# Optimization experiments

Measured on AMD Instinct MI355X. Metric: run time of the kernel, lower is better.

The kernel has to match this reference:

```python
import math
import jax, jax.numpy as jnp
import numpy as np

NUM_HEADS = 16
HEAD_DIM = 128  # hidden_size 2048 / 16 heads


def setup_inputs() -> dict:
    key = jax.random.key(0)
    kq, kk, kv = jax.random.split(key, 3)
    B, S, D = 2, 2048, 2048
    return {
        "query": jax.random.normal(kq, (B, S, D), dtype=jnp.float32),
        "key": jax.random.normal(kk, (B, S, D), dtype=jnp.float32),
        "value": jax.random.normal(kv, (B, S, D), dtype=jnp.float32),
        "attention_mask": jnp.zeros((B, 1, 1, S), dtype=jnp.float32),
    }


def reference(query, key, value, attention_mask):
    B, S, D = query.shape
    H, hd = NUM_HEADS, HEAD_DIM
    # [B, S, D] -> [B, H, S, hd]
    q = query.reshape(B, S, H, hd).transpose(0, 2, 1, 3)
    k = key.reshape(B, S, H, hd).transpose(0, 2, 1, 3)
    v = value.reshape(B, S, H, hd).transpose(0, 2, 1, 3)
    scale = 1.0 / math.sqrt(hd)
    # scores: [B, H, S, S]
    scores = jnp.einsum("bhqd,bhkd->bhqk", q, k) * scale
    scores = scores + attention_mask  # additive broadcastable mask
    attn_weights = jax.nn.softmax(scores, axis=-1)
    # dropout p=0.0 / eval mode -> no-op
    attn_output = jnp.einsum("bhqk,bhkd->bhqd", attn_weights, v)
    attn_output = attn_output.transpose(0, 2, 1, 3).reshape(B, S, D)
    return (attn_output, attn_weights)
```

## Files before the change

kernel.cpp:

```cpp
#include <hip/hip_runtime.h>

#define SQ 2048
#define DM 2048
#define NH 16
#define HD 128
#define NB 2
#define NBH 32

typedef __attribute__((ext_vector_type(8))) short bf16x8;
typedef __attribute__((ext_vector_type(4))) float f32x4;

__device__ __forceinline__ unsigned short f2bf(float f) {
    unsigned u = __float_as_uint(f);
    u += 0x7FFFu + ((u >> 16) & 1u);
    return (unsigned short)(u >> 16);
}
__device__ __forceinline__ float bf2f(unsigned short h) {
    return __uint_as_float(((unsigned)h) << 16);
}

__global__ __launch_bounds__(256) void kconv_kernel(const float* __restrict__ src,
                                                    unsigned short* __restrict__ dst) {
    int e4 = blockIdx.x * 256 + threadIdx.x;
    int d4 = e4 & 31;
    int s  = (e4 >> 5) & (SQ - 1);
    int bh = e4 >> 16;
    int b = bh >> 4, h = bh & 15;
    const float4 v = *(const float4*)(src + ((size_t)(b * SQ + s)) * DM + h * HD + d4 * 4);
    ushort4 o;
    o.x = f2bf(v.x); o.y = f2bf(v.y); o.z = f2bf(v.z); o.w = f2bf(v.w);
    *(ushort4*)(dst + ((size_t)bh * SQ + s) * HD + d4 * 4) = o;
}

__global__ __launch_bounds__(256) void vtrans_kernel(const float* __restrict__ src,
                                                     unsigned short* __restrict__ dst) {
    __shared__ unsigned short tl[128 * 66];
    int bh = blockIdx.x >> 5;
    int s0 = (blockIdx.x & 31) * 64;
    int b = bh >> 4, h = bh & 15;
    #pragma unroll
    for (int i = 0; i < 8; ++i) {
        int e4 = threadIdx.x + 256 * i;
        int d4 = e4 & 31;
        int s  = e4 >> 5;
        const float4 v = *(const float4*)(src + ((size_t)(b * SQ + s0 + s)) * DM + h * HD + d4 * 4);
        tl[(d4 * 4 + 0) * 66 + s] = f2bf(v.x);
        tl[(d4 * 4 + 1) * 66 + s] = f2bf(v.y);
        tl[(d4 * 4 + 2) * 66 + s] = f2bf(v.z);
        tl[(d4 * 4 + 3) * 66 + s] = f2bf(v.w);
    }
    __syncthreads();
    #pragma unroll
    for (int i = 0; i < 16; ++i) {
        int o  = threadIdx.x + 256 * i;
        int d  = o >> 5;
        int s2 = o & 31;
        unsigned u = *(const unsigned*)(tl + d * 66 + s2 * 2);
        *(unsigned*)(dst + ((size_t)(bh * HD + d)) * SQ + s0 + s2 * 2) = u;
    }
}

#define WSTRIDE 2056

__global__ __launch_bounds__(512, 4) void attn_kernel(
    const float* __restrict__ q, const float* __restrict__ mask,
    const unsigned short* __restrict__ kbf, const unsigned short* __restrict__ vt,
    float* __restrict__ outO, float* __restrict__ outW) {

    __shared__ __align__(16) unsigned short q_lds[16 * 136];
    __shared__ __align__(16) unsigned short w_lds[16 * WSTRIDE];
    __shared__ float red_s[8][16];
    __shared__ float rlrow[16];

    const int tid = threadIdx.x;
    const int bh = blockIdx.x >> 7;
    const int q0 = (blockIdx.x & 127) << 4;
    const int b = bh >> 4, h = bh & 15;

    {
        int row = tid >> 5, c4 = tid & 31;
        const float4 v = *(const float4*)(q + ((size_t)(b * SQ + q0 + row)) * DM + h * HD + c4 * 4);
        ushort4 o; o.x = f2bf(v.x); o.y = f2bf(v.y); o.z = f2bf(v.z); o.w = f2bf(v.w);
        *(ushort4*)(q_lds + row * 136 + c4 * 4) = o;
    }
    __syncthreads();

    const int wave = tid >> 6, lane = tid & 63, quad = lane >> 4, ln = lane & 15;
    const float scale = 0.08838834764831845f;

    bf16x8 afr[4];
    #pragma unroll
    for (int ks = 0; ks < 4; ++ks)
        afr[ks] = *(const bf16x8*)(q_lds + ln * 136 + ks * 32 + quad * 8);

    const unsigned short* kb = kbf + (size_t)bh * (SQ * HD);
    const float* mb = mask + b * SQ;
    float rs0 = 0.f, rs1 = 0.f, rs2 = 0.f, rs3 = 0.f;
    for (int it = 0; it < 16; ++it) {
        int n0 = it * 128 + wave * 16;
        f32x4 acc = {0.f, 0.f, 0.f, 0.f};
        const unsigned short* kr = kb + (size_t)(n0 + ln) * HD + quad * 8;
        #pragma unroll
        for (int ks = 0; ks < 4; ++ks) {
            bf16x8 bfr = *(const bf16x8*)(kr + ks * 32);
            acc = __builtin_amdgcn_mfma_f32_16x16x32_bf16(afr[ks], bfr, acc, 0, 0, 0);
        }
        float mv = mb[n0 + ln];
        float e0 = __expf(acc[0] * scale + mv);
        float e1 = __expf(acc[1] * scale + mv);
        float e2 = __expf(acc[2] * scale + mv);
        float e3 = __expf(acc[3] * scale + mv);
        rs0 += e0; rs1 += e1; rs2 += e2; rs3 += e3;
        unsigned short* wp = w_lds + (quad * 4) * WSTRIDE + n0 + ln;
        wp[0 * WSTRIDE] = f2bf(e0);
        wp[1 * WSTRIDE] = f2bf(e1);
        wp[2 * WSTRIDE] = f2bf(e2);
        wp[3 * WSTRIDE] = f2bf(e3);
    }
    rs0 += __shfl_xor(rs0, 1); rs0 += __shfl_xor(rs0, 2); rs0 += __shfl_xor(rs0, 4); rs0 += __shfl_xor(rs0, 8);
    rs1 += __shfl_xor(rs1, 1); rs1 += __shfl_xor(rs1, 2); rs1 += __shfl_xor(rs1, 4); rs1 += __shfl_xor(rs1, 8);
    rs2 += __shfl_xor(rs2, 1); rs2 += __shfl_xor(rs2, 2); rs2 += __shfl_xor(rs2, 4); rs2 += __shfl_xor(rs2, 8);
    rs3 += __shfl_xor(rs3, 1); rs3 += __shfl_xor(rs3, 2); rs3 += __shfl_xor(rs3, 4); rs3 += __shfl_xor(rs3, 8);
    if (ln == 0) {
        red_s[wave][quad * 4 + 0] = rs0;
        red_s[wave][quad * 4 + 1] = rs1;
        red_s[wave][quad * 4 + 2] = rs2;
        red_s[wave][quad * 4 + 3] = rs3;
    }
    __syncthreads();

    if (tid < 16) {
        float l = 0.f;
        #pragma unroll
        for (int w = 0; w < 8; ++w) l += red_s[w][tid];
        rlrow[tid] = 1.0f / l;
    }
    __syncthreads();

    float* wbase = outW + ((size_t)bh * SQ + q0) * SQ;
    for (int i = 0; i < 16; ++i) {
        int e4 = tid + 512 * i;
        int rr = e4 >> 9;
        int c4 = (e4 & 511) * 4;
        float rl = rlrow[rr];
        ushort4 u = *(ushort4*)(w_lds + rr * WSTRIDE + c4);
        f32x4 w;
        w[0] = bf2f(u.x) * rl; w[1] = bf2f(u.y) * rl;
        w[2] = bf2f(u.z) * rl; w[3] = bf2f(u.w) * rl;
        __builtin_nontemporal_store(w, (f32x4*)(wbase + (size_t)rr * SQ + c4));
    }

    {
        int d0 = wave * 16;
        f32x4 o0 = {0.f, 0.f, 0.f, 0.f};
        const unsigned short* vb = vt + (size_t)bh * (HD * SQ);
        const unsigned short* vp = vb + (size_t)(d0 + ln) * SQ + quad * 8;
        const unsigned short* ap = w_lds + ln * WSTRIDE + quad * 8;
        for (int kk = 0; kk < 64; ++kk) {
            bf16x8 a  = *(const bf16x8*)(ap + kk * 32);
            bf16x8 b0 = *(const bf16x8*)(vp + kk * 32);
            o0 = __builtin_amdgcn_mfma_f32_16x16x32_bf16(a, b0, o0, 0, 0, 0);
        }
        float* ob = outO + ((size_t)(b * SQ + q0)) * DM + h * HD;
        #pragma unroll
        for (int r = 0; r < 4; ++r) {
            int row = quad * 4 + r;
            ob[(size_t)row * DM + d0 + ln] = o0[r] * rlrow[row];
        }
    }
}

extern "C" void kernel_launch(void* const* d_in, const int* in_sizes, int n_in,
                              void* d_out, int out_size, void* d_ws, size_t ws_size,
                              hipStream_t stream) {
    const float* q    = (const float*)d_in[0];
    const float* k    = (const float*)d_in[1];
    const float* v    = (const float*)d_in[2];
    const float* mask = (const float*)d_in[3];

    float* outO = (float*)d_out;
    float* outW = outO + (size_t)NB * SQ * DM;

    const size_t elems = (size_t)NBH * SQ * HD;
    if (ws_size < 2 * elems * sizeof(unsigned short)) return;
    unsigned short* kbf = (unsigned short*)d_ws;
    unsigned short* vtp = kbf + elems;

    kconv_kernel<<<8192, 256, 0, stream>>>(k, kbf);
    vtrans_kernel<<<1024, 256, 0, stream>>>(v, vtp);
    attn_kernel<<<4096, 512, 0, stream>>>(q, mask, kbf, vtp, outO, outW);
}
```

Baseline: 988.1 us.

## Split waves between weight stores and PV matmul, swizzle blocks, double QK accumulators

Blocks are remapped so that consecutive workgroups go to different heads and query tiles. The QK loop now computes two 16-column MFMA tiles per iteration to expose more independent work. After the softmax reduction, waves 0-3 write the normalized attention weights to global memory while waves 4-7 run the PV MFMA with two accumulators each, so the large weight stores overlap with the matmul. Each wave recomputes the row reciprocals locally, which removes one barrier. The store half now has only four waves issuing writes, which may limit store bandwidth.

```diff
diff --git a/kernel.cpp b/kernel.cpp
--- a/kernel.cpp
+++ b/kernel.cpp
@@ -70,11 +70,11 @@
     __shared__ __align__(16) unsigned short q_lds[16 * 136];
     __shared__ __align__(16) unsigned short w_lds[16 * WSTRIDE];
     __shared__ float red_s[8][16];
-    __shared__ float rlrow[16];
 
     const int tid = threadIdx.x;
-    const int bh = blockIdx.x >> 7;
-    const int q0 = (blockIdx.x & 127) << 4;
+    const int lb = (blockIdx.x & 7) * 512 + (blockIdx.x >> 3);
+    const int bh = lb >> 7;
+    const int q0 = (lb & 127) << 4;
     const int b = bh >> 4, h = bh & 15;
 
     {
@@ -96,26 +96,33 @@
     const unsigned short* kb = kbf + (size_t)bh * (SQ * HD);
     const float* mb = mask + b * SQ;
     float rs0 = 0.f, rs1 = 0.f, rs2 = 0.f, rs3 = 0.f;
-    for (int it = 0; it < 16; ++it) {
-        int n0 = it * 128 + wave * 16;
-        f32x4 acc = {0.f, 0.f, 0.f, 0.f};
-        const unsigned short* kr = kb + (size_t)(n0 + ln) * HD + quad * 8;
+    for (int it = 0; it < 8; ++it) {
+        int n0 = it * 256 + wave * 16;
+        f32x4 accA = {0.f, 0.f, 0.f, 0.f};
+        f32x4 accB = {0.f, 0.f, 0.f, 0.f};
+        const unsigned short* krA = kb + (size_t)(n0 + ln) * HD + quad * 8;
+        const unsigned short* krB = krA + (size_t)128 * HD;
         #pragma unroll
         for (int ks = 0; ks < 4; ++ks) {
-            bf16x8 bfr = *(const bf16x8*)(kr + ks * 32);
-            acc = __builtin_amdgcn_mfma_f32_16x16x32_bf16(afr[ks], bfr, acc, 0, 0, 0);
-        }
-        float mv = mb[n0 + ln];
-        float e0 = __expf(acc[0] * scale + mv);
-        float e1 = __expf(acc[1] * scale + mv);
-        float e2 = __expf(acc[2] * scale + mv);
-        float e3 = __expf(acc[3] * scale + mv);
-        rs0 += e0; rs1 += e1; rs2 += e2; rs3 += e3;
-        unsigned short* wp = w_lds + (quad * 4) * WSTRIDE + n0 + ln;
-        wp[0 * WSTRIDE] = f2bf(e0);
-        wp[1 * WSTRIDE] = f2bf(e1);
-        wp[2 * WSTRIDE] = f2bf(e2);
-        wp[3 * WSTRIDE] = f2bf(e3);
+            bf16x8 ba = *(const bf16x8*)(krA + ks * 32);
+            bf16x8 bb = *(const bf16x8*)(krB + ks * 32);
+            accA = __builtin_amdgcn_mfma_f32_16x16x32_bf16(afr[ks], ba, accA, 0, 0, 0);
+            accB = __builtin_amdgcn_mfma_f32_16x16x32_bf16(afr[ks], bb, accB, 0, 0, 0);
+        }
+        float mvA = mb[n0 + ln];
+        float mvB = mb[n0 + 128 + ln];
+        unsigned short* wpA = w_lds + (quad * 4) * WSTRIDE + n0 + ln;
+        #pragma unroll
+        for (int r = 0; r < 4; ++r) {
+            float eA = __expf(accA[r] * scale + mvA);
+            float eB = __expf(accB[r] * scale + mvB);
+            if (r == 0) { rs0 += eA + eB; }
+            else if (r == 1) { rs1 += eA + eB; }
+            else if (r == 2) { rs2 += eA + eB; }
+            else { rs3 += eA + eB; }
+            wpA[r * WSTRIDE]       = f2bf(eA);
+            wpA[r * WSTRIDE + 128] = f2bf(eB);
+        }
     }
     rs0 += __shfl_xor(rs0, 1); rs0 += __shfl_xor(rs0, 2); rs0 += __shfl_xor(rs0, 4); rs0 += __shfl_xor(rs0, 8);
     rs1 += __shfl_xor(rs1, 1); rs1 += __shfl_xor(rs1, 2); rs1 += __shfl_xor(rs1, 4); rs1 += __shfl_xor(rs1, 8);
@@ -129,43 +136,56 @@
     }
     __syncthreads();
 
-    if (tid < 16) {
-        float l = 0.f;
-        #pragma unroll
-        for (int w = 0; w < 8; ++w) l += red_s[w][tid];
-        rlrow[tid] = 1.0f / l;
-    }
-    __syncthreads();
-
-    float* wbase = outW + ((size_t)bh * SQ + q0) * SQ;
-    for (int i = 0; i < 16; ++i) {
-        int e4 = tid + 512 * i;
-        int rr = e4 >> 9;
-        int c4 = (e4 & 511) * 4;
-        float rl = rlrow[rr];
-        ushort4 u = *(ushort4*)(w_lds + rr * WSTRIDE + c4);
-        f32x4 w;
-        w[0] = bf2f(u.x) * rl; w[1] = bf2f(u.y) * rl;
-        w[2] = bf2f(u.z) * rl; w[3] = bf2f(u.w) * rl;
-        __builtin_nontemporal_store(w, (f32x4*)(wbase + (size_t)rr * SQ + c4));
-    }
-
-    {
-        int d0 = wave * 16;
-        f32x4 o0 = {0.f, 0.f, 0.f, 0.f};
-        const unsigned short* vb = vt + (size_t)bh * (HD * SQ);
-        const unsigned short* vp = vb + (size_t)(d0 + ln) * SQ + quad * 8;
-        const unsigned short* ap = w_lds + ln * WSTRIDE + quad * 8;
+    if (wave < 4) {
+        float rl4[4];
+        #pragma unroll
+        for (int j = 0; j < 4; ++j) {
+            float l = 0.f;
+            #pragma unroll
+            for (int wv = 0; wv < 8; ++wv) l += red_s[wv][wave * 4 + j];
+            rl4[j] = 1.0f / l;
+        }
+        float* wbase = outW + ((size_t)bh * SQ + q0) * SQ;
+        #pragma unroll
+        for (int i = 0; i < 32; ++i) {
+            int row = wave * 4 + (i >> 3);
+            int col = (i & 7) * 256 + lane * 4;
+            float rl = rl4[i >> 3];
+            ushort4 u = *(ushort4*)(w_lds + row * WSTRIDE + col);
+            f32x4 w;
+            w[0] = bf2f(u.x) * rl; w[1] = bf2f(u.y) * rl;
+            w[2] = bf2f(u.z) * rl; w[3] = bf2f(u.w) * rl;
+            __builtin_nontemporal_store(w, (f32x4*)(wbase + (size_t)row * SQ + col));
+        }
+    } else {
+        int d0 = (wave - 4) * 32;
+        f32x4 o0 = {0.f, 0.f, 0.f, 0.f}, o1 = {0.f, 0.f, 0.f, 0.f};
+        const unsigned short* vb  = vt + (size_t)bh * (HD * SQ);
+        const unsigned short* v0p = vb + (size_t)(d0 + ln) * SQ + quad * 8;
+        const unsigned short* v1p = v0p + (size_t)16 * SQ;
+        const unsigned short* ap  = w_lds + ln * WSTRIDE + quad * 8;
+        #pragma unroll 4
         for (int kk = 0; kk < 64; ++kk) {
             bf16x8 a  = *(const bf16x8*)(ap + kk * 32);
-            bf16x8 b0 = *(const bf16x8*)(vp + kk * 32);
+            bf16x8 b0 = *(const bf16x8*)(v0p + kk * 32);
+            bf16x8 b1 = *(const bf16x8*)(v1p + kk * 32);
             o0 = __builtin_amdgcn_mfma_f32_16x16x32_bf16(a, b0, o0, 0, 0, 0);
+            o1 = __builtin_amdgcn_mfma_f32_16x16x32_bf16(a, b1, o1, 0, 0, 0);
+        }
+        float rl4[4];
+        #pragma unroll
+        for (int r = 0; r < 4; ++r) {
+            float l = 0.f;
+            #pragma unroll
+            for (int wv = 0; wv < 8; ++wv) l += red_s[wv][quad * 4 + r];
+            rl4[r] = 1.0f / l;
         }
         float* ob = outO + ((size_t)(b * SQ + q0)) * DM + h * HD;
         #pragma unroll
         for (int r = 0; r < 4; ++r) {
             int row = quad * 4 + r;
-            ob[(size_t)row * DM + d0 + ln] = o0[r] * rlrow[row];
+            ob[(size_t)row * DM + d0 + ln]      = o0[r] * rl4[r];
+            ob[(size_t)row * DM + d0 + 16 + ln] = o1[r] * rl4[r];
         }
     }
 }
```

After: 0.9999 ms. Within noise of the previous version (+1.2%).
